# Kernel optimization log

Hardware: AMD Instinct MI355X
Metric: run time of the kernel (lower is better)

The kernel has to match this reference:

```python
import jax, jax.numpy as jnp
import numpy as np

DIM = 512
DIM_TIME = 64
DIM_FF = 2048
B, L = 2, 512
EPS = 1e-5


def _layer_norm(x, g, b):
    mu = jnp.mean(x, axis=-1, keepdims=True)
    var = jnp.mean((x - mu) ** 2, axis=-1, keepdims=True)
    return (x - mu) * jax.lax.rsqrt(var + EPS) * g + b


def _sioconv(u, wa, hid_re, hid_im):
    # u: (B, L, Dt) float. Faithful to the FFT/triu construction, expressed as
    # cumulative log-sums (linear conv with all-ones == causal cumsum).
    Bb, Ll, Dt = u.shape
    out = (u @ wa.T).reshape(Bb, Ll, Dt, 2)          # linear_a, view_as_complex
    a_sqr = out[..., 0] ** 2 + out[..., 1] ** 2
    a = (out[..., 0] + 1j * out[..., 1]) * (jax.lax.rsqrt(a_sqr) * jnp.exp(-a_sqr))
    a = jnp.transpose(a, (0, 2, 1))                  # (B, Dt, L)
    a_ln = jnp.log(a)
    S = jnp.cumsum(a_ln, axis=-1)                    # S_k = sum_{j<=k} ln a_j
    S_prev = jnp.concatenate([jnp.zeros_like(S[..., :1]), S[..., :-1]], axis=-1)
    # c[b,d,i,k] = exp(S_k - S_{i-1}) = prod_{j=i..k} a_j, kept for k >= i-1
    diff = S[:, :, None, :] - S_prev[:, :, :, None]  # (B, Dt, L, L)
    idx = jnp.arange(Ll)
    mask = idx[None, :] >= (idx[:, None] - 1)        # k >= i-1 (triu diag=-1)
    c = jnp.where(mask, jnp.exp(diff), 0.0)
    uc = jnp.transpose(u.astype(jnp.complex64), (0, 2, 1))   # (B, Dt, L)
    hidden = (hid_re + 1j * hid_im)[None, :] * jnp.ones((Bb, 1), jnp.complex64)
    xin = jnp.concatenate([hidden[..., None], uc[..., :-1]], axis=-1)  # rolled + h0
    h = jnp.einsum('bdik,bdk->bdi', c, xin)
    h = h.at[:, :, -1].add(uc[:, :, -1])
    return jnp.transpose(h.real, (0, 2, 1)).astype(u.dtype)


def _ffn(x, w1, b1, w2, b2):
    return jax.nn.silu(x @ w1.T + b1) @ w2.T + b2


def setup_inputs() -> dict:
    key = jax.random.key(0)
    ks = jax.random.split(key, 12)
    d, dt, dff = DIM, DIM_TIME, DIM_FF
    return {
        'x': jax.random.normal(ks[0], (B, L, d), jnp.float32),
        'ln1_g': jnp.ones((d,), jnp.float32), 'ln1_b': jnp.zeros((d,), jnp.float32),
        'fc_w': jax.random.normal(ks[1], (dt, d), jnp.float32) * d ** -0.5,
        'fc_b': jnp.zeros((dt,), jnp.float32),
        'lin_in_w': jax.random.normal(ks[2], (dt, d), jnp.float32) * d ** -0.5,
        'lin_in_b': jnp.zeros((dt,), jnp.float32),
        'wa': jax.random.normal(ks[3], (2 * dt, dt), jnp.float32) * dt ** -0.5,
        'hid_re': jax.random.normal(ks[4], (dt,), jnp.float32),
        'hid_im': jax.random.normal(ks[5], (dt,), jnp.float32),
        'lin_out_w': jax.random.normal(ks[6], (d, dt), jnp.float32) * dt ** -0.5,
        'lin_out_b': jnp.zeros((d,), jnp.float32),
        'ln2_g': jnp.ones((d,), jnp.float32), 'ln2_b': jnp.zeros((d,), jnp.float32),
        'w1': jax.random.normal(ks[7], (dff, d), jnp.float32) * d ** -0.5,
        'b1': jnp.zeros((dff,), jnp.float32),
        'w2': jax.random.normal(ks[8], (d, dff), jnp.float32) * dff ** -0.5,
        'b2': jnp.zeros((d,), jnp.float32),
    }


def reference(x, ln1_g, ln1_b, fc_w, fc_b, lin_in_w, lin_in_b, wa, hid_re, hid_im,
              lin_out_w, lin_out_b, ln2_g, ln2_b, w1, b1, w2, b2):
    x_res = x
    xn = _layer_norm(x, ln1_g, ln1_b)
    y = jax.nn.silu(xn @ fc_w.T + fc_b)                  # gate, (B, L, Dt)
    u = xn @ lin_in_w.T + lin_in_b                       # (B, L, Dt)
    h = _sioconv(u, wa, hid_re, hid_im)
    x = (h * y) @ lin_out_w.T + lin_out_b + x_res        # dropout = identity (eval)
    x_res = x
    x = _ffn(_layer_norm(x, ln2_g, ln2_b), w1, b1, w2, b2) + x_res
    return x
```

## Files before the change

### kernel.cpp

```cpp
#include <hip/hip_runtime.h>
#include <math.h>

#define LSEQ 512
#define DMODEL 512
#define DT 64
#define DFF 2048

typedef unsigned short u16;
typedef __attribute__((ext_vector_type(8))) short short8;
typedef __attribute__((ext_vector_type(4))) float f32x4;
typedef __attribute__((ext_vector_type(16))) float f32x16;

__device__ __forceinline__ float wave_sum(float v) {
#pragma unroll
  for (int o = 32; o > 0; o >>= 1) v += __shfl_xor(v, o, 64);
  return v;
}

__device__ __forceinline__ u16 f2bf(float f) {
  unsigned int u = __float_as_uint(f);
  u += 0x7fffu + ((u >> 16) & 1u);
  return (u16)(u >> 16);
}
__device__ __forceinline__ float bf2f(u16 h) {
  return __uint_as_float(((unsigned int)h) << 16);
}
__device__ __forceinline__ void splitbf(float f, u16& h, u16& l) {
  h = f2bf(f);
  l = f2bf(f - bf2f(h));
}
__device__ __forceinline__ void split8(const float* __restrict__ p,
                                       short8& bh, short8& bl) {
  float4 a = *(const float4*)p;
  float4 b = *(const float4*)(p + 4);
  float vv[8] = {a.x, a.y, a.z, a.w, b.x, b.y, b.z, b.w};
#pragma unroll
  for (int e = 0; e < 8; ++e) {
    u16 h, l; splitbf(vv[e], h, l);
    bh[e] = (short)h; bl[e] = (short)l;
  }
}


__global__ __launch_bounds__(512) void k_fa(
    const float* __restrict__ x, const float* __restrict__ g1,
    const float* __restrict__ be1,
    const float* __restrict__ fcw, const float* __restrict__ liw,
    const float* __restrict__ wa,
    const float* __restrict__ fcb, const float* __restrict__ lib,
    const float* __restrict__ w1, const float* __restrict__ w2,
    float* __restrict__ y_o, float* __restrict__ u_o,
    float* __restrict__ ar_o, float* __restrict__ ai_o,
    u16* __restrict__ w1s, u16* __restrict__ w2s)
{
  const int blk = blockIdx.x;
  if (blk >= 64) {
    for (int i = (blk - 64) * 512 + threadIdx.x; i < 524288; i += 131072) {
      if (i < 262144) {
        int r = i >> 7, c0 = (i & 127) << 2;
        float4 v = ((const float4*)w1)[i];
        ushort4 o;
        o.x = f2bf(v.x); o.y = f2bf(v.y); o.z = f2bf(v.z); o.w = f2bf(v.w);
        int flat = (r >> 4) * 8192 + (c0 >> 5) * 512 +
                   ((r & 15) + 16 * ((c0 & 31) >> 3)) * 8 + (c0 & 7);
        *(ushort4*)(w1s + flat) = o;
      } else {
        int ii = i - 262144;
        int r = ii >> 9, c0 = (ii & 511) << 2;
        float4 v = ((const float4*)w2)[ii];
        ushort4 o;
        o.x = f2bf(v.x); o.y = f2bf(v.y); o.z = f2bf(v.z); o.w = f2bf(v.w);
        int lane_s = (r & 31) + (((c0 & 15) >> 3) << 5);
        int flat = (r >> 5) * 65536 + (c0 >> 4) * 512 + lane_s * 8 + (c0 & 7);
        *(ushort4*)(w2s + flat) = o;
      }
    }
    return;
  }
  __shared__ __align__(16) u16 xsh[16][520];
  __shared__ __align__(16) u16 xsl[16][520];
  __shared__ __align__(16) u16 ush[16][80];
  __shared__ __align__(16) u16 usl[16][80];
  const int tid = threadIdx.x;
  const int wv = tid >> 6, lane = tid & 63;
  const int lr = lane & 15, lk = lane >> 4;
  const int mt = blk;

#pragma unroll
  for (int rr = 0; rr < 2; ++rr) {
    const int r = wv * 2 + rr;
    const int row = mt * 16 + r;
    const float* xr = x + (size_t)row * DMODEL;
    float v[8]; float s = 0.f;
#pragma unroll
    for (int j = 0; j < 8; ++j) { v[j] = xr[lane + 64 * j]; s += v[j]; }
    s = wave_sum(s);
    const float mu = s * (1.f / 512.f);
    float q = 0.f;
#pragma unroll
    for (int j = 0; j < 8; ++j) { float dd = v[j] - mu; q += dd * dd; }
    q = wave_sum(q);
    const float rstd = rsqrtf(q * (1.f / 512.f) + 1e-5f);
#pragma unroll
    for (int j = 0; j < 8; ++j) {
      int idx = lane + 64 * j;
      float o = (v[j] - mu) * rstd * g1[idx] + be1[idx];
      u16 h, l; splitbf(o, h, l);
      xsh[r][idx] = h;
      xsl[r][idx] = l;
    }
  }
  __syncthreads();

  const int c = wv * 16 + lr;
  {
    const float* brow = (c < DT) ? (fcw + (size_t)c * DMODEL)
                                 : (liw + (size_t)(c - DT) * DMODEL);
    f32x4 acc = {};
#pragma unroll 4
    for (int k = 0; k < DMODEL; k += 32) {
      short8 ah = *(const short8*)&xsh[lr][k + lk * 8];
      short8 al = *(const short8*)&xsl[lr][k + lk * 8];
      short8 bh, bl;
      split8(brow + k + lk * 8, bh, bl);
      acc = __builtin_amdgcn_mfma_f32_16x16x32_bf16(ah, bh, acc, 0, 0, 0);
      acc = __builtin_amdgcn_mfma_f32_16x16x32_bf16(ah, bl, acc, 0, 0, 0);
      acc = __builtin_amdgcn_mfma_f32_16x16x32_bf16(al, bh, acc, 0, 0, 0);
    }
#pragma unroll
    for (int j = 0; j < 4; ++j) {
      int rl = lk * 4 + j;
      int row = mt * 16 + rl;
      float v = acc[j];
      if (c < DT) {
        v += fcb[c];
        y_o[row * DT + c] = v / (1.f + expf(-v));
      } else {
        int d = c - DT;
        v += lib[d];
        u_o[row * DT + d] = v;
        u16 h, l; splitbf(v, h, l);
        ush[rl][d] = h; usl[rl][d] = l;
      }
    }
  }
  __syncthreads();
  {
    const float* warow = wa + (size_t)c * DT;
    f32x4 acc = {};
#pragma unroll
    for (int ks = 0; ks < 2; ++ks) {
      short8 ah = *(const short8*)&ush[lr][ks * 32 + lk * 8];
      short8 al = *(const short8*)&usl[lr][ks * 32 + lk * 8];
      short8 bh, bl;
      split8(warow + ks * 32 + lk * 8, bh, bl);
      acc = __builtin_amdgcn_mfma_f32_16x16x32_bf16(ah, bh, acc, 0, 0, 0);
      acc = __builtin_amdgcn_mfma_f32_16x16x32_bf16(ah, bl, acc, 0, 0, 0);
      acc = __builtin_amdgcn_mfma_f32_16x16x32_bf16(al, bh, acc, 0, 0, 0);
    }
#pragma unroll
    for (int j = 0; j < 4; ++j) {
      float v = acc[j];
      float p = __shfl_xor(v, 1, 64);
      float re = (lane & 1) ? p : v;
      float im = (lane & 1) ? v : p;
      float asq = re * re + im * im;
      float sc = rsqrtf(asq) * expf(-asq);
      int row = mt * 16 + lk * 4 + j;
      int d = c >> 1;
      if (lane & 1) ai_o[row * DT + d] = im * sc;
      else          ar_o[row * DT + d] = re * sc;
    }
  }
}

__global__ __launch_bounds__(64) void k_scan2(
    const float* __restrict__ u, const float* __restrict__ ar, const float* __restrict__ ai,
    const float* __restrict__ hr, const float* __restrict__ hi, float* __restrict__ h_o)
{
  const int blk = blockIdx.x;
  const int b = blk >> 6, d = blk & 63;
  const int lane = threadIdx.x;
  const size_t base = (size_t)b * LSEQ * DT + d;
  const int i0 = lane * 8;

  float a_r[8], a_i[8], b_r[8], b_i[8];
#pragma unroll
  for (int e = 0; e < 8; ++e) {
    int i = i0 + e;
    a_r[e] = ar[base + (size_t)i * DT];
    a_i[e] = ai[base + (size_t)i * DT];
    if (i >= 2)      { b_r[e] = u[base + (size_t)(i - 2) * DT]; b_i[e] = 0.f; }
    else if (i == 1) { b_r[e] = hr[d]; b_i[e] = hi[d]; }
    else             { b_r[e] = 0.f;   b_i[e] = 0.f; }
  }

  float Ar = 1.f, Ai = 0.f, Br = 0.f, Bi = 0.f;
#pragma unroll
  for (int e = 0; e < 8; ++e) {
    float nBr = fmaf(Ar, b_r[e], fmaf(-Ai, b_i[e], Br));
    float nBi = fmaf(Ar, b_i[e], fmaf( Ai, b_r[e], Bi));
    float nAr = Ar * a_r[e] - Ai * a_i[e];
    float nAi = Ar * a_i[e] + Ai * a_r[e];
    Ar = nAr; Ai = nAi; Br = nBr; Bi = nBi;
  }

#pragma unroll
  for (int dlt = 1; dlt < 64; dlt <<= 1) {
    float Ar2 = __shfl_down(Ar, dlt, 64);
    float Ai2 = __shfl_down(Ai, dlt, 64);
    float Br2 = __shfl_down(Br, dlt, 64);
    float Bi2 = __shfl_down(Bi, dlt, 64);
    if (lane + dlt < 64) {
      float nAr = Ar * Ar2 - Ai * Ai2;
      float nAi = Ar * Ai2 + Ai * Ar2;
      float nBr = fmaf(Ar, Br2, fmaf(-Ai, Bi2, Br));
      float nBi = fmaf(Ar, Bi2, fmaf( Ai, Br2, Bi));
      Ar = nAr; Ai = nAi; Br = nBr; Bi = nBi;
    }
  }

  float A1r = __shfl_down(Ar, 1, 64), A1i = __shfl_down(Ai, 1, 64);
  float B1r = __shfl_down(Br, 1, 64), B1i = __shfl_down(Bi, 1, 64);
  if (lane == 63) { A1r = 1.f; A1i = 0.f; B1r = 0.f; B1i = 0.f; }
  const float r512 = u[base + (size_t)(LSEQ - 2) * DT];
  float rr = fmaf(A1r, r512, B1r);
  float ri = fmaf(A1i, r512, B1i);

  const float uL = u[base + (size_t)(LSEQ - 1) * DT];
#pragma unroll
  for (int e = 7; e >= 0; --e) {
    int i = i0 + e;
    float nr = fmaf(a_r[e], rr, fmaf(-a_i[e], ri, b_r[e]));
    float ni = fmaf(a_r[e], ri, fmaf( a_i[e], rr, b_i[e]));
    rr = nr; ri = ni;
    float outv = rr;
    if (i == LSEQ - 1) outv += uL;
    h_o[base + (size_t)i * DT] = outv;
  }
}

__global__ __launch_bounds__(512) void k_mfl(
    const float* __restrict__ h, const float* __restrict__ y,
    const float* __restrict__ low, const float* __restrict__ lob,
    const float* __restrict__ x, const float* __restrict__ g2,
    const float* __restrict__ be2, const float* __restrict__ b1,
    const u16* __restrict__ w1s,
    float* __restrict__ x2_o, u16* __restrict__ h1s)
{
  __shared__ __align__(16) u16 hyh[16][80];
  __shared__ __align__(16) u16 hyl[16][80];
  __shared__ float x2s[16][520];
  __shared__ __align__(16) u16 xn2[16][520];
  const int tid = threadIdx.x;
  const int wv = tid >> 6, lane = tid & 63;
  const int lr = lane & 15, lk = lane >> 4;
  const int mt = blockIdx.x >> 2, chunk = blockIdx.x & 3;

#pragma unroll
  for (int it = 0; it < 2; ++it) {
    int idx = it * 512 + tid;
    int r = idx >> 6, d = idx & 63;
    int row = mt * 16 + r;
    float v = h[row * DT + d] * y[row * DT + d];
    u16 hh, ll; splitbf(v, hh, ll);
    hyh[r][d] = hh; hyl[r][d] = ll;
  }
  __syncthreads();

#pragma unroll
  for (int t = 0; t < 4; ++t) {
    const int nt = wv * 4 + t;
    const float* brow = low + (size_t)(nt * 16 + lr) * DT;
    f32x4 acc = {};
#pragma unroll
    for (int ks = 0; ks < 2; ++ks) {
      short8 ah = *(const short8*)&hyh[lr][ks * 32 + lk * 8];
      short8 al = *(const short8*)&hyl[lr][ks * 32 + lk * 8];
      short8 bh, bl;
      split8(brow + ks * 32 + lk * 8, bh, bl);
      acc = __builtin_amdgcn_mfma_f32_16x16x32_bf16(ah, bh, acc, 0, 0, 0);
      acc = __builtin_amdgcn_mfma_f32_16x16x32_bf16(ah, bl, acc, 0, 0, 0);
      acc = __builtin_amdgcn_mfma_f32_16x16x32_bf16(al, bh, acc, 0, 0, 0);
    }
    const int c = nt * 16 + lr;
#pragma unroll
    for (int j = 0; j < 4; ++j) {
      int rl = lk * 4 + j;
      int row = mt * 16 + rl;
      float v = acc[j] + lob[c] + x[(size_t)row * DMODEL + c];
      x2s[rl][c] = v;
      if (chunk == 0) x2_o[(size_t)row * DMODEL + c] = v;
    }
  }
  __syncthreads();

#pragma unroll
  for (int rr = 0; rr < 2; ++rr) {
    const int r = wv * 2 + rr;
    float v[8]; float s = 0.f;
#pragma unroll
    for (int j = 0; j < 8; ++j) { v[j] = x2s[r][lane + 64 * j]; s += v[j]; }
    s = wave_sum(s);
    const float mu = s * (1.f / 512.f);
    float q = 0.f;
#pragma unroll
    for (int j = 0; j < 8; ++j) { float dd = v[j] - mu; q += dd * dd; }
    q = wave_sum(q);
    const float rstd = rsqrtf(q * (1.f / 512.f) + 1e-5f);
#pragma unroll
    for (int j = 0; j < 8; ++j) {
      int idx = lane + 64 * j;
      xn2[r][idx] = f2bf((v[j] - mu) * rstd * g2[idx] + be2[idx]);
    }
  }
  __syncthreads();

  {
    const int t32 = mt >> 1;
#pragma unroll
    for (int tt = 0; tt < 4; ++tt) {
      const int t = chunk * 32 + wv * 4 + tt;
      const u16* b = w1s + t * 8192 + lane * 8;
      f32x4 acc = {};
#pragma unroll
      for (int kb = 0; kb < 16; ++kb) {
        short8 af = *(const short8*)&xn2[lr][kb * 32 + lk * 8];
        short8 bf = *(const short8*)(b + kb * 512);
        acc = __builtin_amdgcn_mfma_f32_16x16x32_bf16(af, bf, acc, 0, 0, 0);
      }
      const int col = t * 16 + lr;
      const float bb = b1[col];
#pragma unroll
      for (int j = 0; j < 4; ++j) {
        int row16 = lk * 4 + j;
        float v = acc[j] + bb;
        v = v / (1.f + expf(-v));
        int r32 = (mt & 1) * 16 + row16;
        int lane_s = r32 + 32 * (lr >> 3);
        h1s[t32 * 65536 + t * 512 + lane_s * 8 + (lr & 7)] = f2bf(v);
      }
    }
  }
}

__global__ __launch_bounds__(256) void k_ffn2(
    const u16* __restrict__ As, const u16* __restrict__ Bs,
    const float* __restrict__ b2, const float* __restrict__ x2,
    float* __restrict__ out)
{
  __shared__ float red[4][16][64];
  const int w = threadIdx.x >> 6, lane = threadIdx.x & 63;
  const int mt = blockIdx.x, nt = blockIdx.y;
  const u16* a = As + mt * 65536 + w * 32 * 512 + lane * 8;
  const u16* b = Bs + nt * 65536 + w * 32 * 512 + lane * 8;
  f32x16 acc = {};
#pragma unroll 8
  for (int kb = 0; kb < 32; ++kb)
    acc = __builtin_amdgcn_mfma_f32_32x32x16_bf16(*(const short8*)(a + kb * 512),
                                                  *(const short8*)(b + kb * 512),
                                                  acc, 0, 0, 0);
#pragma unroll
  for (int r = 0; r < 16; ++r) red[w][r][lane] = acc[r];
  __syncthreads();
  for (int s = threadIdx.x; s < 1024; s += 256) {
    int r = s >> 6, l = s & 63;
    float v = red[0][r][l] + red[1][r][l] + red[2][r][l] + red[3][r][l];
    int row = mt * 32 + (r & 3) + 8 * (r >> 2) + 4 * (l >> 5);
    int col = nt * 32 + (l & 31);
    out[(size_t)row * DMODEL + col] =
        v + b2[col] + x2[(size_t)row * DMODEL + col];
  }
}

extern "C" void kernel_launch(void* const* d_in, const int* in_sizes, int n_in,
                              void* d_out, int out_size, void* d_ws, size_t ws_size,
                              hipStream_t stream) {
  const float* x    = (const float*)d_in[0];
  const float* ln1g = (const float*)d_in[1];
  const float* ln1b = (const float*)d_in[2];
  const float* fcw  = (const float*)d_in[3];
  const float* fcb  = (const float*)d_in[4];
  const float* liw  = (const float*)d_in[5];
  const float* lib  = (const float*)d_in[6];
  const float* wa   = (const float*)d_in[7];
  const float* hidr = (const float*)d_in[8];
  const float* hidi = (const float*)d_in[9];
  const float* low  = (const float*)d_in[10];
  const float* lob  = (const float*)d_in[11];
  const float* ln2g = (const float*)d_in[12];
  const float* ln2b = (const float*)d_in[13];
  const float* w1   = (const float*)d_in[14];
  const float* b1   = (const float*)d_in[15];
  const float* w2   = (const float*)d_in[16];
  const float* b2   = (const float*)d_in[17];
  float* out = (float*)d_out;
  float* ws  = (float*)d_ws;

  float* y_   = ws;
  float* u_   = y_  + 65536;
  float* ar_  = u_  + 65536;
  float* ai_  = ar_ + 65536;
  float* h_   = ai_ + 65536;
  float* x2_  = h_  + 65536;
  u16* p = (u16*)(x2_ + 524288);
  u16* h1s  = p;            p += 2097152;
  u16* w1s  = p;            p += 1048576;
  u16* w2s  = p;            p += 1048576;

  k_fa<<<320, 512, 0, stream>>>(x, ln1g, ln1b, fcw, liw, wa, fcb, lib, w1, w2,
                                y_, u_, ar_, ai_, w1s, w2s);
  k_scan2<<<128, 64, 0, stream>>>(u_, ar_, ai_, hidr, hidi, h_);
  k_mfl<<<256, 512, 0, stream>>>(h_, y_, low, lob, x, ln2g, ln2b, b1,
                                 w1s, x2_, h1s);
  k_ffn2<<<dim3(32, 16), 256, 0, stream>>>(h1s, w2s, b2, x2_, out);
}
```

Measured before the change: 53.41 us.

## Split K across more waves in input, FFN1 and FFN2 kernels

Measured after the change: 55.71 us. 4.3% more time.

```diff
diff --git a/kernel.cpp b/kernel.cpp
--- a/kernel.cpp
+++ b/kernel.cpp
@@ -9,7 +9,6 @@
 typedef unsigned short u16;
 typedef __attribute__((ext_vector_type(8))) short short8;
 typedef __attribute__((ext_vector_type(4))) float f32x4;
-typedef __attribute__((ext_vector_type(16))) float f32x16;
 
 __device__ __forceinline__ float wave_sum(float v) {
 #pragma unroll
@@ -42,7 +41,7 @@
 }
 
 
-__global__ __launch_bounds__(512) void k_fa(
+__global__ __launch_bounds__(1024) void k_fa(
     const float* __restrict__ x, const float* __restrict__ g1,
     const float* __restrict__ be1,
     const float* __restrict__ fcw, const float* __restrict__ liw,
@@ -54,8 +53,9 @@
     u16* __restrict__ w1s, u16* __restrict__ w2s)
 {
   const int blk = blockIdx.x;
+  const int tid = threadIdx.x;
   if (blk >= 64) {
-    for (int i = (blk - 64) * 512 + threadIdx.x; i < 524288; i += 131072) {
+    for (int i = (blk - 64) * 1024 + tid; i < 524288; i += 131072) {
       if (i < 262144) {
         int r = i >> 7, c0 = (i & 127) << 2;
         float4 v = ((const float4*)w1)[i];
@@ -81,14 +81,13 @@
   __shared__ __align__(16) u16 xsl[16][520];
   __shared__ __align__(16) u16 ush[16][80];
   __shared__ __align__(16) u16 usl[16][80];
-  const int tid = threadIdx.x;
+  __shared__ __align__(16) float pacc[8][2][64][4];
   const int wv = tid >> 6, lane = tid & 63;
   const int lr = lane & 15, lk = lane >> 4;
   const int mt = blk;
 
-#pragma unroll
-  for (int rr = 0; rr < 2; ++rr) {
-    const int r = wv * 2 + rr;
+  {
+    const int r = wv;
     const int row = mt * 16 + r;
     const float* xr = x + (size_t)row * DMODEL;
     float v[8]; float s = 0.f;
@@ -112,26 +111,37 @@
   }
   __syncthreads();
 
-  const int c = wv * 16 + lr;
   {
+    const int t = wv & 7, kh = wv >> 3;
+    const int c = t * 16 + lr;
     const float* brow = (c < DT) ? (fcw + (size_t)c * DMODEL)
                                  : (liw + (size_t)(c - DT) * DMODEL);
+    const int k0 = kh * 256;
     f32x4 acc = {};
 #pragma unroll 4
-    for (int k = 0; k < DMODEL; k += 32) {
-      short8 ah = *(const short8*)&xsh[lr][k + lk * 8];
-      short8 al = *(const short8*)&xsl[lr][k + lk * 8];
+    for (int k = 0; k < 256; k += 32) {
+      short8 ah = *(const short8*)&xsh[lr][k0 + k + lk * 8];
+      short8 al = *(const short8*)&xsl[lr][k0 + k + lk * 8];
       short8 bh, bl;
-      split8(brow + k + lk * 8, bh, bl);
+      split8(brow + k0 + k + lk * 8, bh, bl);
       acc = __builtin_amdgcn_mfma_f32_16x16x32_bf16(ah, bh, acc, 0, 0, 0);
       acc = __builtin_amdgcn_mfma_f32_16x16x32_bf16(ah, bl, acc, 0, 0, 0);
       acc = __builtin_amdgcn_mfma_f32_16x16x32_bf16(al, bh, acc, 0, 0, 0);
     }
+    *(float4*)&pacc[t][kh][lane][0] = float4{acc[0], acc[1], acc[2], acc[3]};
+  }
+  __syncthreads();
+
+  if (wv < 8) {
+    const int c = wv * 16 + lr;
+    float4 p0 = *(const float4*)&pacc[wv][0][lane][0];
+    float4 p1 = *(const float4*)&pacc[wv][1][lane][0];
+    float accv[4] = {p0.x + p1.x, p0.y + p1.y, p0.z + p1.z, p0.w + p1.w};
 #pragma unroll
     for (int j = 0; j < 4; ++j) {
       int rl = lk * 4 + j;
       int row = mt * 16 + rl;
-      float v = acc[j];
+      float v = accv[j];
       if (c < DT) {
         v += fcb[c];
         y_o[row * DT + c] = v / (1.f + expf(-v));
@@ -145,7 +155,8 @@
     }
   }
   __syncthreads();
-  {
+  if (wv < 8) {
+    const int c = wv * 16 + lr;
     const float* warow = wa + (size_t)c * DT;
     f32x4 acc = {};
 #pragma unroll
@@ -255,7 +266,7 @@
   const int tid = threadIdx.x;
   const int wv = tid >> 6, lane = tid & 63;
   const int lr = lane & 15, lk = lane >> 4;
-  const int mt = blockIdx.x >> 2, chunk = blockIdx.x & 3;
+  const int mt = blockIdx.x >> 3, chunk = blockIdx.x & 7;
 
 #pragma unroll
   for (int it = 0; it < 2; ++it) {
@@ -319,8 +330,8 @@
   {
     const int t32 = mt >> 1;
 #pragma unroll
-    for (int tt = 0; tt < 4; ++tt) {
-      const int t = chunk * 32 + wv * 4 + tt;
+    for (int tt = 0; tt < 2; ++tt) {
+      const int t = chunk * 16 + wv * 2 + tt;
       const u16* b = w1s + t * 8192 + lane * 8;
       f32x4 acc = {};
 #pragma unroll
@@ -344,28 +355,31 @@
   }
 }
 
-__global__ __launch_bounds__(256) void k_ffn2(
+__global__ __launch_bounds__(512) void k_ffn2(
     const u16* __restrict__ As, const u16* __restrict__ Bs,
     const float* __restrict__ b2, const float* __restrict__ x2,
     float* __restrict__ out)
 {
-  __shared__ float red[4][16][64];
-  const int w = threadIdx.x >> 6, lane = threadIdx.x & 63;
+  __shared__ float red[8][16][64];
+  const int tid = threadIdx.x;
+  const int w = tid >> 6, lane = tid & 63;
   const int mt = blockIdx.x, nt = blockIdx.y;
-  const u16* a = As + mt * 65536 + w * 32 * 512 + lane * 8;
-  const u16* b = Bs + nt * 65536 + w * 32 * 512 + lane * 8;
+  typedef __attribute__((ext_vector_type(16))) float f32x16;
+  const u16* a = As + mt * 65536 + w * 16 * 512 + lane * 8;
+  const u16* b = Bs + nt * 65536 + w * 16 * 512 + lane * 8;
   f32x16 acc = {};
 #pragma unroll 8
-  for (int kb = 0; kb < 32; ++kb)
+  for (int kb = 0; kb < 16; ++kb)
     acc = __builtin_amdgcn_mfma_f32_32x32x16_bf16(*(const short8*)(a + kb * 512),
                                                   *(const short8*)(b + kb * 512),
                                                   acc, 0, 0, 0);
 #pragma unroll
   for (int r = 0; r < 16; ++r) red[w][r][lane] = acc[r];
   __syncthreads();
-  for (int s = threadIdx.x; s < 1024; s += 256) {
+  for (int s = tid; s < 1024; s += 512) {
     int r = s >> 6, l = s & 63;
-    float v = red[0][r][l] + red[1][r][l] + red[2][r][l] + red[3][r][l];
+    float v = red[0][r][l] + red[1][r][l] + red[2][r][l] + red[3][r][l] +
+              red[4][r][l] + red[5][r][l] + red[6][r][l] + red[7][r][l];
     int row = mt * 32 + (r & 3) + 8 * (r >> 2) + 4 * (l >> 5);
     int col = nt * 32 + (l & 31);
     out[(size_t)row * DMODEL + col] =
@@ -408,10 +422,10 @@
   u16* w1s  = p;            p += 1048576;
   u16* w2s  = p;            p += 1048576;
 
-  k_fa<<<320, 512, 0, stream>>>(x, ln1g, ln1b, fcw, liw, wa, fcb, lib, w1, w2,
-                                y_, u_, ar_, ai_, w1s, w2s);
+  k_fa<<<192, 1024, 0, stream>>>(x, ln1g, ln1b, fcw, liw, wa, fcb, lib, w1, w2,
+                                 y_, u_, ar_, ai_, w1s, w2s);
   k_scan2<<<128, 64, 0, stream>>>(u_, ar_, ai_, hidr, hidi, h_);
-  k_mfl<<<256, 512, 0, stream>>>(h_, y_, low, lob, x, ln2g, ln2b, b1,
+  k_mfl<<<512, 512, 0, stream>>>(h_, y_, low, lob, x, ln2g, ln2b, b1,
                                  w1s, x2_, h1s);
-  k_ffn2<<<dim3(32, 16), 256, 0, stream>>>(h1s, w2s, b2, x2_, out);
-}
+  k_ffn2<<<dim3(32, 16), 512, 0, stream>>>(h1s, w2s, b2, x2_, out);
+}
```
